# Optimization experiments

Measured on AMD Instinct MI355X. Metric: run time of the kernel, lower is better.

The kernel has to match this reference:

```python
import jax, jax.numpy as jnp
import numpy as np

B, D, N, M = 8, 256, 2048, 2048
H = 4
DH = D // H  # 64
EPS = 1e-5


def setup_inputs() -> dict:
    key = jax.random.key(0)
    ks = jax.random.split(key, 16)
    s = 0.05
    return {
        "x": jax.random.normal(ks[0], (B, D, N), jnp.float32),
        "source": jax.random.normal(ks[1], (B, D, M), jnp.float32),
        # per-head QKV projection weights (equivalent to H separate Conv1d(D, DH, 1))
        "Wq": jax.random.normal(ks[2], (H, DH, D), jnp.float32) * s,
        "bq": jax.random.normal(ks[3], (H, DH), jnp.float32) * s,
        "Wk": jax.random.normal(ks[4], (H, DH, D), jnp.float32) * s,
        "bk": jax.random.normal(ks[5], (H, DH), jnp.float32) * s,
        "Wv": jax.random.normal(ks[6], (H, DH, D), jnp.float32) * s,
        "bv": jax.random.normal(ks[7], (H, DH), jnp.float32) * s,
        # merge Conv1d(D, D, 1)
        "Wm": jax.random.normal(ks[8], (D, D), jnp.float32) * s,
        "bm": jax.random.normal(ks[9], (D,), jnp.float32) * s,
        # MLP: Conv1d(2D, 2D, 1) -> InstanceNorm -> ReLU -> Conv1d(2D, D, 1)
        "W1": jax.random.normal(ks[10], (2 * D, 2 * D), jnp.float32) * s,
        "b1": jax.random.normal(ks[11], (2 * D,), jnp.float32) * s,
        "W2": jax.random.normal(ks[12], (D, 2 * D), jnp.float32) * s,
        "b2": jnp.zeros((D,), jnp.float32),  # nn.init.constant_(mlp[-1].bias, 0.0)
    }


def reference(x, source, Wq, bq, Wk, bk, Wv, bv, Wm, bm, W1, b1, W2, b2):
    # Per-head 1x1-conv QKV projections, batched: [B, DH, H, N]
    q = jnp.einsum('bdn,hkd->bkhn', x, Wq) + bq.T[None, :, :, None]
    k = jnp.einsum('bdm,hkd->bkhm', source, Wk) + bk.T[None, :, :, None]
    v = jnp.einsum('bdm,hkd->bkhm', source, Wv) + bv.T[None, :, :, None]
    # scaled dot-product attention (scale = head dim)
    scores = jnp.einsum('bkhn,bkhm->bhnm', q, k) / jnp.sqrt(jnp.float32(DH))
    prob = jax.nn.softmax(scores, axis=-1)
    msg = jnp.einsum('bhnm,bkhm->bkhn', prob, v)
    # view(B, DH*H, N): dim-major then head, matches jnp reshape of [B, DH, H, N]
    msg = msg.reshape(B, DH * H, N)
    message = jnp.einsum('bcn,ec->ben', msg, Wm) + bm[None, :, None]
    # MLP on concat([x, message])
    h = jnp.concatenate([x, message], axis=1)  # [B, 2D, N]
    h = jnp.einsum('bcn,oc->bon', h, W1) + b1[None, :, None]
    # InstanceNorm1d (affine=False, biased variance, eps=1e-5) over N per (b, c)
    mean = jnp.mean(h, axis=-1, keepdims=True)
    var = jnp.var(h, axis=-1, keepdims=True)
    h = (h - mean) / jnp.sqrt(var + EPS)
    h = jax.nn.relu(h)
    out = jnp.einsum('bcn,oc->bon', h, W2) + b2[None, :, None]
    return out
```

## Files before the change

kernel.cpp:

```cpp
#include <hip/hip_runtime.h>
#include <hip/hip_bf16.h>

#define B_  8
#define D_  256
#define N_  2048
#define M_  2048
#define H_  4
#define DH_ 64
#define D2_ 512

#define SCL_QK 0.1803368801f

typedef unsigned short ushort_t;
typedef __attribute__((ext_vector_type(8))) short bf16x8;
typedef __attribute__((ext_vector_type(4))) short bf16x4;
typedef __attribute__((ext_vector_type(4))) float f32x4;

__device__ __forceinline__ unsigned cvtpk(float a, float b) {
  unsigned r;
  asm("v_cvt_pk_bf16_f32 %0, %1, %2" : "=v"(r) : "v"(a), "v"(b));
  return r;
}
__device__ __forceinline__ ushort_t f2bf1(float x) {
  return (ushort_t)cvtpk(x, x);
}
__device__ __forceinline__ float bf2f(ushort_t h) {
  union { unsigned u; float f; } c; c.u = ((unsigned)h) << 16; return c.f;
}
__device__ __forceinline__ uint2 pack4(float a, float b, float c, float d) {
  uint2 r; r.x = cvtpk(a, b); r.y = cvtpk(c, d); return r;
}

__device__ __forceinline__ void gload16(const ushort_t* g, ushort_t* l) {
  __builtin_amdgcn_global_load_lds(
      (const __attribute__((address_space(1))) unsigned*)g,
      (__attribute__((address_space(3))) unsigned*)l, 16, 0, 0);
}

template <int K, int LDB>
__device__ __forceinline__ void mfma_core(const ushort_t* __restrict__ Arow,
                                          const ushort_t* __restrict__ Brow,
                                          f32x4 acc[4][4], int lg) {
#pragma unroll 2
  for (int k0 = 0; k0 < K; k0 += 32) {
    bf16x8 af[4], bfr[4];
#pragma unroll
    for (int f = 0; f < 4; ++f)
      af[f] = *(const bf16x8*)&Arow[(size_t)16 * f * K + k0 + lg * 8];
#pragma unroll
    for (int f = 0; f < 4; ++f)
      bfr[f] = *(const bf16x8*)&Brow[(size_t)16 * f * LDB + k0 + lg * 8];
#pragma unroll
    for (int fm = 0; fm < 4; ++fm)
#pragma unroll
      for (int fn = 0; fn < 4; ++fn)
        acc[fm][fn] = __builtin_amdgcn_mfma_f32_16x16x32_bf16(
            af[fm], bfr[fn], acc[fm][fn], 0, 0, 0);
  }
}

#define GEMM_PREAMBLE()                                   \
  const int t = threadIdx.x, lane = t & 63, wv = t >> 6;  \
  const int wm = wv >> 1, wn = wv & 1;                    \
  const int lq = lane & 15, lg = lane >> 4;               \
  const int m0 = blockIdx.y * 128 + wm * 64;              \
  const int n0 = blockIdx.x * 128 + wn * 64;              \
  f32x4 acc[4][4];                                        \
  _Pragma("unroll") for (int i = 0; i < 4; ++i)           \
  _Pragma("unroll") for (int j = 0; j < 4; ++j)           \
      acc[i][j] = (f32x4){0.f, 0.f, 0.f, 0.f};

__global__ __launch_bounds__(256) void prep_weights(
    const float* __restrict__ Wq, const float* __restrict__ Wk,
    const float* __restrict__ Wv, const float* __restrict__ Wm,
    const float* __restrict__ W1, const float* __restrict__ W2,
    ushort_t* __restrict__ Wqb, ushort_t* __restrict__ Wkb,
    ushort_t* __restrict__ Wvb, ushort_t* __restrict__ Wmb,
    ushort_t* __restrict__ W1b, ushort_t* __restrict__ W2b) {
  const int idx = blockIdx.x * 256 + threadIdx.x;
  if (idx < 65536) {
    Wqb[idx] = f2bf1(Wq[idx] * SCL_QK);
  } else if (idx < 131072) {
    int j = idx - 65536; Wkb[j] = f2bf1(Wk[j]);
  } else if (idx < 196608) {
    int j = idx - 131072; Wvb[j] = f2bf1(Wv[j]);
  } else if (idx < 262144) {
    int j = idx - 196608;
    int e = j >> 8, cp = j & 255;
    int h = cp >> 6, dh = cp & 63;
    Wmb[j] = f2bf1(Wm[e * 256 + dh * 4 + h]);
  } else if (idx < 524288) {
    int j = idx - 262144; W1b[j] = f2bf1(W1[j]);
  } else if (idx < 655360) {
    int j = idx - 524288; W2b[j] = f2bf1(W2[j]);
  }
}

__global__ __launch_bounds__(256) void transpose_in(
    const float* __restrict__ x, const float* __restrict__ source,
    ushort_t* __restrict__ cat_t, ushort_t* __restrict__ st) {
  __shared__ float T[64][65];
  const int t = threadIdx.x;
  const int b = blockIdx.z & 7, which = blockIdx.z >> 3;
  const float* sb = (which ? source : x) + (size_t)b * D_ * N_;
  ushort_t* dst = which ? st + (size_t)b * N_ * 256 : cat_t + (size_t)b * N_ * 512;
  const int ldc = which ? 256 : 512;
  const int d0 = blockIdx.y * 64, n0 = blockIdx.x * 64;
  const int nn = t & 63, dd = t >> 6;
#pragma unroll
  for (int p = 0; p < 16; ++p)
    T[dd + 4 * p][nn] = sb[(size_t)(d0 + dd + 4 * p) * N_ + n0 + nn];
  __syncthreads();
  const int dg = t & 7, nr = t >> 3;
#pragma unroll
  for (int p = 0; p < 2; ++p) {
    int n = nr + 32 * p;
    uint4 pv;
    pv.x = cvtpk(T[dg * 8 + 0][n], T[dg * 8 + 1][n]);
    pv.y = cvtpk(T[dg * 8 + 2][n], T[dg * 8 + 3][n]);
    pv.z = cvtpk(T[dg * 8 + 4][n], T[dg * 8 + 5][n]);
    pv.w = cvtpk(T[dg * 8 + 6][n], T[dg * 8 + 7][n]);
    *(uint4*)&dst[(size_t)(n0 + n) * ldc + d0 + dg * 8] = pv;
  }
}

__global__ __launch_bounds__(256) void q_mfma(
    const ushort_t* __restrict__ Wqb, const float* __restrict__ bq,
    const ushort_t* __restrict__ cat_t, ushort_t* __restrict__ Qt) {
  GEMM_PREAMBLE()
  const int b = blockIdx.z;
  const ushort_t* Arow = Wqb + (size_t)(m0 + lq) * 256;
  const ushort_t* Brow = cat_t + ((size_t)b * N_ + n0 + lq) * 512;
  mfma_core<256, 512>(Arow, Brow, acc, lg);
  ushort_t* Qb = Qt + (size_t)b * 4 * N_ * 64;
#pragma unroll
  for (int fm = 0; fm < 4; ++fm) {
    const int o0 = m0 + 16 * fm + 4 * lg;
    const int hh = o0 >> 6, dl = o0 & 63;
    float bb[4];
#pragma unroll
    for (int r = 0; r < 4; ++r) bb[r] = bq[o0 + r] * SCL_QK;
#pragma unroll
    for (int fn = 0; fn < 4; ++fn) {
      const int n = n0 + 16 * fn + lq;
      uint2 pv = pack4(acc[fm][fn][0] + bb[0], acc[fm][fn][1] + bb[1],
                       acc[fm][fn][2] + bb[2], acc[fm][fn][3] + bb[3]);
      *(uint2*)&Qb[((size_t)hh * N_ + n) * 64 + dl] = pv;
    }
  }
}

__global__ __launch_bounds__(256) void kv_mfma(
    const ushort_t* __restrict__ Wkb, const ushort_t* __restrict__ Wvb,
    const float* __restrict__ bk, const float* __restrict__ bv,
    const ushort_t* __restrict__ st, ushort_t* __restrict__ Kt,
    ushort_t* __restrict__ Vt) {
  const int b = blockIdx.z >> 1, w = blockIdx.z & 1;
  GEMM_PREAMBLE()
  const ushort_t* A = w ? Wvb : Wkb;
  const float* bias = w ? bv : bk;
  const ushort_t* Arow = A + (size_t)(m0 + lq) * 256;
  const ushort_t* Brow = st + ((size_t)b * N_ + n0 + lq) * 256;
  mfma_core<256, 256>(Arow, Brow, acc, lg);
  if (w == 0) {
    ushort_t* Kb = Kt + (size_t)b * 4 * N_ * 64;
#pragma unroll
    for (int fm = 0; fm < 4; ++fm) {
      const int o0 = m0 + 16 * fm + 4 * lg;
      const int hh = o0 >> 6, dl = o0 & 63;
      float bb[4];
#pragma unroll
      for (int r = 0; r < 4; ++r) bb[r] = bias[o0 + r];
#pragma unroll
      for (int fn = 0; fn < 4; ++fn) {
        const int n = n0 + 16 * fn + lq;
        uint2 pv = pack4(acc[fm][fn][0] + bb[0], acc[fm][fn][1] + bb[1],
                         acc[fm][fn][2] + bb[2], acc[fm][fn][3] + bb[3]);
        *(uint2*)&Kb[((size_t)hh * N_ + n) * 64 + dl] = pv;
      }
    }
  } else {
    ushort_t* Vb = Vt + (size_t)b * 256 * N_;
#pragma unroll
    for (int fm = 0; fm < 4; ++fm) {
      const int o0 = m0 + 16 * fm + 4 * lg;
      float bb[4];
#pragma unroll
      for (int r = 0; r < 4; ++r) bb[r] = bias[o0 + r];
#pragma unroll
      for (int fn = 0; fn < 4; ++fn) {
        const int n = n0 + 16 * fn + lq;
#pragma unroll
        for (int r = 0; r < 4; ++r)
          Vb[(size_t)(o0 + r) * N_ + n] = f2bf1(acc[fm][fn][r] + bb[r]);
      }
    }
  }
}

__global__ __launch_bounds__(256) void attn_mfma(
    const ushort_t* __restrict__ Qt, const ushort_t* __restrict__ Kt,
    const ushort_t* __restrict__ Vt, ushort_t* __restrict__ msgT) {
  __shared__ __align__(16) ushort_t Ks[2 * 64 * 64];
  __shared__ __align__(16) ushort_t Vs[2 * 64 * 64];
  __shared__ __align__(16) ushort_t Ps[64 * 64];
  const int t = threadIdx.x;
  const int lane = t & 63, wq = t >> 6;
  const int flat = blockIdx.x;
  const int logical = (flat & 7) * 128 + (flat >> 3);
  const int qt = logical & 31, h = (logical >> 5) & 3, b = logical >> 7;
  const int bh = b * H_ + h;
  const size_t base = (size_t)bh * 64 * N_;
  const int n00 = qt * 64;
  const int lq = lane & 15, lg = lane >> 4;
  const int qrow = wq * 16 + lq;
  const int sw = (lq & 7) * 8;

  const int r0 = wq * 16 + (lane >> 3);
  const int r1 = r0 + 8;
  const int c8 = lane & 7;
  const ushort_t* kp0 = Kt + base + (size_t)r0 * 64 + ((c8 ^ (r0 & 7)) * 8);
  const ushort_t* kp1 = Kt + base + (size_t)r1 * 64 + ((c8 ^ (r1 & 7)) * 8);
  const ushort_t* vp0 = Vt + base + (size_t)r0 * N_ + ((c8 ^ (r0 & 7)) * 8);
  const ushort_t* vp1 = Vt + base + (size_t)r1 * N_ + ((c8 ^ (r1 & 7)) * 8);
  const int wbase = wq * 1024;

  bf16x8 qf0, qf1;
  {
    const ushort_t* qp = Qt + base + (size_t)(n00 + qrow) * 64 + lg * 8;
    qf0 = *(const bf16x8*)qp;
    qf1 = *(const bf16x8*)(qp + 32);
  }
  f32x4 o0 = {0.f, 0.f, 0.f, 0.f}, o1 = o0, o2 = o0, o3 = o0;
  float lrun = 0.f;

  gload16(kp0, &Ks[wbase]);
  gload16(kp1, &Ks[wbase + 512]);
  gload16(vp0, &Vs[wbase]);
  gload16(vp1, &Vs[wbase + 512]);
  kp0 += 4096; kp1 += 4096; vp0 += 64; vp1 += 64;
  __syncthreads();

  int cur = 0;
  for (int tile = 0; tile < 32; ++tile) {
    if (tile != 31) {
      const int nb = (cur ^ 1) * 4096;
      gload16(kp0, &Ks[nb + wbase]);
      gload16(kp1, &Ks[nb + wbase + 512]);
      gload16(vp0, &Vs[nb + wbase]);
      gload16(vp1, &Vs[nb + wbase + 512]);
      kp0 += 4096; kp1 += 4096; vp0 += 64; vp1 += 64;
    }
    const int kb = cur * 4096;

    f32x4 s0 = {0.f, 0.f, 0.f, 0.f}, s1 = s0, s2 = s0, s3 = s0;
#pragma unroll
    for (int kt = 0; kt < 2; ++kt) {
      const int dh0 = ((lg * 8 + 32 * kt) ^ sw) + kb;
      const bf16x8 qb = kt ? qf1 : qf0;
      s0 = __builtin_amdgcn_mfma_f32_16x16x32_bf16(
          *(const bf16x8*)&Ks[lq * 64 + dh0], qb, s0, 0, 0, 0);
      s1 = __builtin_amdgcn_mfma_f32_16x16x32_bf16(
          *(const bf16x8*)&Ks[(16 + lq) * 64 + dh0], qb, s1, 0, 0, 0);
      s2 = __builtin_amdgcn_mfma_f32_16x16x32_bf16(
          *(const bf16x8*)&Ks[(32 + lq) * 64 + dh0], qb, s2, 0, 0, 0);
      s3 = __builtin_amdgcn_mfma_f32_16x16x32_bf16(
          *(const bf16x8*)&Ks[(48 + lq) * 64 + dh0], qb, s3, 0, 0, 0);
    }

    float ls = 0.f;
#define PSTORE(SF, KF)                                                    \
    {                                                                     \
      float e0 = exp2f(SF[0]), e1 = exp2f(SF[1]);                         \
      float e2 = exp2f(SF[2]), e3 = exp2f(SF[3]);                         \
      ls += (e0 + e1) + (e2 + e3);                                        \
      uint2 pv;                                                           \
      pv.x = cvtpk(e0, e1);                                               \
      pv.y = cvtpk(e2, e3);                                               \
      *(uint2*)&Ps[qrow * 64 + ((16 * (KF) + 4 * lg) ^ sw)] = pv;         \
    }
    PSTORE(s0, 0) PSTORE(s1, 1) PSTORE(s2, 2) PSTORE(s3, 3)
#undef PSTORE
    lrun += ls;
    asm volatile("s_waitcnt lgkmcnt(0)" ::: "memory");
    __builtin_amdgcn_sched_barrier(0);

#pragma unroll
    for (int kt = 0; kt < 2; ++kt) {
      const int k0 = (lg * 8 + 32 * kt) ^ sw;
      const bf16x8 pb = *(const bf16x8*)&Ps[qrow * 64 + k0];
      o0 = __builtin_amdgcn_mfma_f32_16x16x32_bf16(
          *(const bf16x8*)&Vs[lq * 64 + k0 + kb], pb, o0, 0, 0, 0);
      o1 = __builtin_amdgcn_mfma_f32_16x16x32_bf16(
          *(const bf16x8*)&Vs[(16 + lq) * 64 + k0 + kb], pb, o1, 0, 0, 0);
      o2 = __builtin_amdgcn_mfma_f32_16x16x32_bf16(
          *(const bf16x8*)&Vs[(32 + lq) * 64 + k0 + kb], pb, o2, 0, 0, 0);
      o3 = __builtin_amdgcn_mfma_f32_16x16x32_bf16(
          *(const bf16x8*)&Vs[(48 + lq) * 64 + k0 + kb], pb, o3, 0, 0, 0);
    }
    __syncthreads();
    cur ^= 1;
  }

  lrun += __shfl_xor(lrun, 16);
  lrun += __shfl_xor(lrun, 32);
  const float inv = 1.f / lrun;

  ushort_t* mp = msgT + ((size_t)b * N_ + n00 + qrow) * 256 + h * 64;
  uint2 pv;
  pv = pack4(o0[0] * inv, o0[1] * inv, o0[2] * inv, o0[3] * inv);
  *(uint2*)&mp[0 + 4 * lg] = pv;
  pv = pack4(o1[0] * inv, o1[1] * inv, o1[2] * inv, o1[3] * inv);
  *(uint2*)&mp[16 + 4 * lg] = pv;
  pv = pack4(o2[0] * inv, o2[1] * inv, o2[2] * inv, o2[3] * inv);
  *(uint2*)&mp[32 + 4 * lg] = pv;
  pv = pack4(o3[0] * inv, o3[1] * inv, o3[2] * inv, o3[3] * inv);
  *(uint2*)&mp[48 + 4 * lg] = pv;
}

__global__ __launch_bounds__(256) void merge_mfma(
    const ushort_t* __restrict__ Wmb, const float* __restrict__ bm,
    const ushort_t* __restrict__ msgT, ushort_t* __restrict__ cat_t) {
  GEMM_PREAMBLE()
  const int b = blockIdx.z;
  const ushort_t* Arow = Wmb + (size_t)(m0 + lq) * 256;
  const ushort_t* Brow = msgT + ((size_t)b * N_ + n0 + lq) * 256;
  mfma_core<256, 256>(Arow, Brow, acc, lg);
  ushort_t* ob = cat_t + (size_t)b * N_ * 512 + 256;
#pragma unroll
  for (int fm = 0; fm < 4; ++fm) {
    const int o0 = m0 + 16 * fm + 4 * lg;
    float bb[4];
#pragma unroll
    for (int r = 0; r < 4; ++r) bb[r] = bm[o0 + r];
#pragma unroll
    for (int fn = 0; fn < 4; ++fn) {
      const int n = n0 + 16 * fn + lq;
      uint2 pv = pack4(acc[fm][fn][0] + bb[0], acc[fm][fn][1] + bb[1],
                       acc[fm][fn][2] + bb[2], acc[fm][fn][3] + bb[3]);
      *(uint2*)&ob[(size_t)n * 512 + o0] = pv;
    }
  }
}

__global__ __launch_bounds__(256) void w1_mfma(
    const ushort_t* __restrict__ W1b, const float* __restrict__ b1,
    const ushort_t* __restrict__ cat_t, ushort_t* __restrict__ h1t) {
  GEMM_PREAMBLE()
  const int b = blockIdx.z;
  const ushort_t* Arow = W1b + (size_t)(m0 + lq) * 512;
  const ushort_t* Brow = cat_t + ((size_t)b * N_ + n0 + lq) * 512;
  mfma_core<512, 512>(Arow, Brow, acc, lg);
  ushort_t* ob = h1t + (size_t)b * N_ * 512;
#pragma unroll
  for (int fm = 0; fm < 4; ++fm) {
    const int o0 = m0 + 16 * fm + 4 * lg;
    float bb[4];
#pragma unroll
    for (int r = 0; r < 4; ++r) bb[r] = b1[o0 + r];
#pragma unroll
    for (int fn = 0; fn < 4; ++fn) {
      const int n = n0 + 16 * fn + lq;
      uint2 pv = pack4(acc[fm][fn][0] + bb[0], acc[fm][fn][1] + bb[1],
                       acc[fm][fn][2] + bb[2], acc[fm][fn][3] + bb[3]);
      *(uint2*)&ob[(size_t)n * 512 + o0] = pv;
    }
  }
}

__global__ __launch_bounds__(256) void zero_stats(float* __restrict__ s) {
  s[blockIdx.x * 256 + threadIdx.x] = 0.f;
}

__global__ __launch_bounds__(256) void stats_partial(
    const ushort_t* __restrict__ h1t, float* __restrict__ ssum,
    float* __restrict__ ssq) {
  const int t = threadIdx.x;
  const int c = blockIdx.y * 64 + (t & 63);
  const int b = blockIdx.z;
  const int nbase = blockIdx.x * 256 + (t >> 6) * 64;
  const ushort_t* p = h1t + (size_t)b * N_ * 512;
  float s = 0.f, ss = 0.f;
  for (int i = 0; i < 64; ++i) {
    float v = bf2f(p[(size_t)(nbase + i) * 512 + c]);
    s += v; ss += v * v;
  }
  __shared__ float rs[4][64], rq[4][64];
  const int wv = t >> 6;
  rs[wv][t & 63] = s; rq[wv][t & 63] = ss;
  __syncthreads();
  if (t < 64) {
    float S = rs[0][t] + rs[1][t] + rs[2][t] + rs[3][t];
    float Q = rq[0][t] + rq[1][t] + rq[2][t] + rq[3][t];
    atomicAdd(&ssum[b * 512 + blockIdx.y * 64 + t], S);
    atomicAdd(&ssq[b * 512 + blockIdx.y * 64 + t], Q);
  }
}

__global__ __launch_bounds__(256) void finalize_stats(
    const float* __restrict__ ssum, const float* __restrict__ ssq,
    float* __restrict__ mean, float* __restrict__ istd) {
  const int i = blockIdx.x * 256 + threadIdx.x;
  float mn = ssum[i] * (1.f / N_);
  float var = ssq[i] * (1.f / N_) - mn * mn;
  mean[i] = mn;
  istd[i] = rsqrtf(var + 1e-5f);
}

__global__ __launch_bounds__(256) void normalize_h1(
    const ushort_t* __restrict__ h1t, const float* __restrict__ mean,
    const float* __restrict__ istd, ushort_t* __restrict__ h1n) {
  const size_t ci = (size_t)blockIdx.x * 256 + threadIdx.x;
  const size_t basei = ci * 8;
  const int c0 = (int)(basei & 511);
  const size_t row = basei >> 9;
  const int b = (int)(row >> 11);
  const float* mp = mean + b * 512 + c0;
  const float* ip = istd + b * 512 + c0;
  union { bf16x8 v; ushort_t u[8]; } in;
  in.v = *(const bf16x8*)&h1t[basei];
  float g[8];
#pragma unroll
  for (int j = 0; j < 8; ++j)
    g[j] = fmaxf((bf2f(in.u[j]) - mp[j]) * ip[j], 0.f);
  uint4 pv;
  pv.x = cvtpk(g[0], g[1]);
  pv.y = cvtpk(g[2], g[3]);
  pv.z = cvtpk(g[4], g[5]);
  pv.w = cvtpk(g[6], g[7]);
  *(uint4*)&h1n[basei] = pv;
}

__global__ __launch_bounds__(256) void w2_mfma(
    const ushort_t* __restrict__ W2b, const float* __restrict__ b2,
    const ushort_t* __restrict__ h1n, float* __restrict__ out) {
  GEMM_PREAMBLE()
  const int b = blockIdx.z;
  const ushort_t* Arow = W2b + (size_t)(m0 + lq) * 512;
  const ushort_t* Brow = h1n + ((size_t)b * N_ + n0 + lq) * 512;
  mfma_core<512, 512>(Arow, Brow, acc, lg);
  float* ob = out + (size_t)b * D_ * N_;
#pragma unroll
  for (int fm = 0; fm < 4; ++fm) {
    const int o0 = m0 + 16 * fm + 4 * lg;
    float bb[4];
#pragma unroll
    for (int r = 0; r < 4; ++r) bb[r] = b2[o0 + r];
#pragma unroll
    for (int fn = 0; fn < 4; ++fn) {
      const int n = n0 + 16 * fn + lq;
#pragma unroll
      for (int r = 0; r < 4; ++r)
        ob[(size_t)(o0 + r) * N_ + n] = acc[fm][fn][r] + bb[r];
    }
  }
}

extern "C" void kernel_launch(void* const* d_in, const int* in_sizes, int n_in,
                              void* d_out, int out_size, void* d_ws,
                              size_t ws_size, hipStream_t stream) {
  const float* x = (const float*)d_in[0];
  const float* source = (const float*)d_in[1];
  const float* Wq = (const float*)d_in[2];
  const float* bq = (const float*)d_in[3];
  const float* Wk = (const float*)d_in[4];
  const float* bk = (const float*)d_in[5];
  const float* Wv = (const float*)d_in[6];
  const float* bv = (const float*)d_in[7];
  const float* Wm = (const float*)d_in[8];
  const float* bm = (const float*)d_in[9];
  const float* W1 = (const float*)d_in[10];
  const float* b1 = (const float*)d_in[11];
  const float* W2 = (const float*)d_in[12];
  const float* b2 = (const float*)d_in[13];
  float* out = (float*)d_out;

  char* w = (char*)d_ws;
  size_t off = 0;
  auto alloc = [&](size_t bytes) {
    void* p = w + off;
    off = (off + bytes + 255) & ~(size_t)255;
    return p;
  };
  ushort_t* cat_t = (ushort_t*)alloc((size_t)B_ * N_ * 512 * 2);
  ushort_t* st    = (ushort_t*)alloc((size_t)B_ * N_ * 256 * 2);
  ushort_t* Qt    = (ushort_t*)alloc((size_t)B_ * 4 * N_ * 64 * 2);
  ushort_t* Kt    = (ushort_t*)alloc((size_t)B_ * 4 * N_ * 64 * 2);
  ushort_t* Vt    = (ushort_t*)alloc((size_t)B_ * 256 * N_ * 2);
  ushort_t* msgT  = (ushort_t*)alloc((size_t)B_ * N_ * 256 * 2);
  ushort_t* h1t   = (ushort_t*)alloc((size_t)B_ * N_ * 512 * 2);
  ushort_t* h1n   = (ushort_t*)alloc((size_t)B_ * N_ * 512 * 2);
  float* ssum = (float*)alloc(4096 * 4);
  float* ssq  = (float*)alloc(4096 * 4);
  float* mean = (float*)alloc(4096 * 4);
  float* istd = (float*)alloc(4096 * 4);
  ushort_t* Wqb = (ushort_t*)alloc(65536 * 2);
  ushort_t* Wkb = (ushort_t*)alloc(65536 * 2);
  ushort_t* Wvb = (ushort_t*)alloc(65536 * 2);
  ushort_t* Wmb = (ushort_t*)alloc(65536 * 2);
  ushort_t* W1b = (ushort_t*)alloc(262144 * 2);
  ushort_t* W2b = (ushort_t*)alloc(131072 * 2);

  prep_weights<<<2560, 256, 0, stream>>>(Wq, Wk, Wv, Wm, W1, W2, Wqb, Wkb,
                                         Wvb, Wmb, W1b, W2b);
  transpose_in<<<dim3(32, 4, 16), 256, 0, stream>>>(x, source, cat_t, st);
  zero_stats<<<32, 256, 0, stream>>>(ssum);
  q_mfma<<<dim3(16, 2, 8), 256, 0, stream>>>(Wqb, bq, cat_t, Qt);
  kv_mfma<<<dim3(16, 2, 16), 256, 0, stream>>>(Wkb, Wvb, bk, bv, st, Kt, Vt);
  attn_mfma<<<dim3(1024), 256, 0, stream>>>(Qt, Kt, Vt, msgT);
  merge_mfma<<<dim3(16, 2, 8), 256, 0, stream>>>(Wmb, bm, msgT, cat_t);
  w1_mfma<<<dim3(16, 4, 8), 256, 0, stream>>>(W1b, b1, cat_t, h1t);
  stats_partial<<<dim3(8, 8, 8), 256, 0, stream>>>(h1t, ssum, ssq);
  finalize_stats<<<16, 256, 0, stream>>>(ssum, ssq, mean, istd);
  normalize_h1<<<4096, 256, 0, stream>>>(h1t, mean, istd, h1n);
  w2_mfma<<<dim3(16, 2, 8), 256, 0, stream>>>(W2b, b2, h1n, out);
}
```

Before: 286.9 us.

## Fuse QKV projections and move instance-norm statistics into W1 GEMM epilogue

Merges the Q and KV projection kernels into one launch, folds stats zeroing into the weight prep kernel, and computes per-channel sum and sum-of-squares inside the W1 GEMM epilogue via shuffles and atomics. The finalize step is folded into the normalize kernel. This removes several kernel launches and a full re-read of the h1 activation. It adds atomic traffic per block and computes statistics from fp32 values rather than the rounded bf16 ones.

```diff
diff --git a/kernel.cpp b/kernel.cpp
--- a/kernel.cpp
+++ b/kernel.cpp
@@ -70,13 +70,14 @@
   _Pragma("unroll") for (int j = 0; j < 4; ++j)           \
       acc[i][j] = (f32x4){0.f, 0.f, 0.f, 0.f};
 
-__global__ __launch_bounds__(256) void prep_weights(
+__global__ __launch_bounds__(256) void prep_kernel(
     const float* __restrict__ Wq, const float* __restrict__ Wk,
     const float* __restrict__ Wv, const float* __restrict__ Wm,
     const float* __restrict__ W1, const float* __restrict__ W2,
     ushort_t* __restrict__ Wqb, ushort_t* __restrict__ Wkb,
     ushort_t* __restrict__ Wvb, ushort_t* __restrict__ Wmb,
-    ushort_t* __restrict__ W1b, ushort_t* __restrict__ W2b) {
+    ushort_t* __restrict__ W1b, ushort_t* __restrict__ W2b,
+    float* __restrict__ stats) {
   const int idx = blockIdx.x * 256 + threadIdx.x;
   if (idx < 65536) {
     Wqb[idx] = f2bf1(Wq[idx] * SCL_QK);
@@ -93,6 +94,9 @@
     int j = idx - 262144; W1b[j] = f2bf1(W1[j]);
   } else if (idx < 655360) {
     int j = idx - 524288; W2b[j] = f2bf1(W2[j]);
+  } else {
+    int j = idx - 655360;
+    if (j < 8192) stats[j] = 0.f;
   }
 }
 
@@ -124,53 +128,48 @@
   }
 }
 
-__global__ __launch_bounds__(256) void q_mfma(
-    const ushort_t* __restrict__ Wqb, const float* __restrict__ bq,
-    const ushort_t* __restrict__ cat_t, ushort_t* __restrict__ Qt) {
+__global__ __launch_bounds__(256) void qkv_mfma(
+    const ushort_t* __restrict__ Wqb, const ushort_t* __restrict__ Wkb,
+    const ushort_t* __restrict__ Wvb, const float* __restrict__ bq,
+    const float* __restrict__ bk, const float* __restrict__ bv,
+    const ushort_t* __restrict__ cat_t, const ushort_t* __restrict__ st,
+    ushort_t* __restrict__ Qt, ushort_t* __restrict__ Kt,
+    ushort_t* __restrict__ Vt) {
+  const int z = blockIdx.z;
+  const int b = z / 3, w = z % 3;
   GEMM_PREAMBLE()
-  const int b = blockIdx.z;
-  const ushort_t* Arow = Wqb + (size_t)(m0 + lq) * 256;
-  const ushort_t* Brow = cat_t + ((size_t)b * N_ + n0 + lq) * 512;
-  mfma_core<256, 512>(Arow, Brow, acc, lg);
-  ushort_t* Qb = Qt + (size_t)b * 4 * N_ * 64;
-#pragma unroll
-  for (int fm = 0; fm < 4; ++fm) {
-    const int o0 = m0 + 16 * fm + 4 * lg;
-    const int hh = o0 >> 6, dl = o0 & 63;
-    float bb[4];
-#pragma unroll
-    for (int r = 0; r < 4; ++r) bb[r] = bq[o0 + r] * SCL_QK;
-#pragma unroll
-    for (int fn = 0; fn < 4; ++fn) {
-      const int n = n0 + 16 * fn + lq;
-      uint2 pv = pack4(acc[fm][fn][0] + bb[0], acc[fm][fn][1] + bb[1],
-                       acc[fm][fn][2] + bb[2], acc[fm][fn][3] + bb[3]);
-      *(uint2*)&Qb[((size_t)hh * N_ + n) * 64 + dl] = pv;
-    }
-  }
-}
-
-__global__ __launch_bounds__(256) void kv_mfma(
-    const ushort_t* __restrict__ Wkb, const ushort_t* __restrict__ Wvb,
-    const float* __restrict__ bk, const float* __restrict__ bv,
-    const ushort_t* __restrict__ st, ushort_t* __restrict__ Kt,
-    ushort_t* __restrict__ Vt) {
-  const int b = blockIdx.z >> 1, w = blockIdx.z & 1;
-  GEMM_PREAMBLE()
-  const ushort_t* A = w ? Wvb : Wkb;
-  const float* bias = w ? bv : bk;
-  const ushort_t* Arow = A + (size_t)(m0 + lq) * 256;
-  const ushort_t* Brow = st + ((size_t)b * N_ + n0 + lq) * 256;
-  mfma_core<256, 256>(Arow, Brow, acc, lg);
   if (w == 0) {
-    ushort_t* Kb = Kt + (size_t)b * 4 * N_ * 64;
+    const ushort_t* Arow = Wqb + (size_t)(m0 + lq) * 256;
+    const ushort_t* Brow = cat_t + ((size_t)b * N_ + n0 + lq) * 512;
+    mfma_core<256, 512>(Arow, Brow, acc, lg);
+    ushort_t* Qb = Qt + (size_t)b * 4 * N_ * 64;
 #pragma unroll
     for (int fm = 0; fm < 4; ++fm) {
       const int o0 = m0 + 16 * fm + 4 * lg;
       const int hh = o0 >> 6, dl = o0 & 63;
       float bb[4];
 #pragma unroll
-      for (int r = 0; r < 4; ++r) bb[r] = bias[o0 + r];
+      for (int r = 0; r < 4; ++r) bb[r] = bq[o0 + r] * SCL_QK;
+#pragma unroll
+      for (int fn = 0; fn < 4; ++fn) {
+        const int n = n0 + 16 * fn + lq;
+        uint2 pv = pack4(acc[fm][fn][0] + bb[0], acc[fm][fn][1] + bb[1],
+                         acc[fm][fn][2] + bb[2], acc[fm][fn][3] + bb[3]);
+        *(uint2*)&Qb[((size_t)hh * N_ + n) * 64 + dl] = pv;
+      }
+    }
+  } else if (w == 1) {
+    const ushort_t* Arow = Wkb + (size_t)(m0 + lq) * 256;
+    const ushort_t* Brow = st + ((size_t)b * N_ + n0 + lq) * 256;
+    mfma_core<256, 256>(Arow, Brow, acc, lg);
+    ushort_t* Kb = Kt + (size_t)b * 4 * N_ * 64;
+#pragma unroll
+    for (int fm = 0; fm < 4; ++fm) {
+      const int o0 = m0 + 16 * fm + 4 * lg;
+      const int hh = o0 >> 6, dl = o0 & 63;
+      float bb[4];
+#pragma unroll
+      for (int r = 0; r < 4; ++r) bb[r] = bk[o0 + r];
 #pragma unroll
       for (int fn = 0; fn < 4; ++fn) {
         const int n = n0 + 16 * fn + lq;
@@ -180,13 +179,16 @@
       }
     }
   } else {
+    const ushort_t* Arow = Wvb + (size_t)(m0 + lq) * 256;
+    const ushort_t* Brow = st + ((size_t)b * N_ + n0 + lq) * 256;
+    mfma_core<256, 256>(Arow, Brow, acc, lg);
     ushort_t* Vb = Vt + (size_t)b * 256 * N_;
 #pragma unroll
     for (int fm = 0; fm < 4; ++fm) {
       const int o0 = m0 + 16 * fm + 4 * lg;
       float bb[4];
 #pragma unroll
-      for (int r = 0; r < 4; ++r) bb[r] = bias[o0 + r];
+      for (int r = 0; r < 4; ++r) bb[r] = bv[o0 + r];
 #pragma unroll
       for (int fn = 0; fn < 4; ++fn) {
         const int n = n0 + 16 * fn + lq;
@@ -345,7 +347,8 @@
 
 __global__ __launch_bounds__(256) void w1_mfma(
     const ushort_t* __restrict__ W1b, const float* __restrict__ b1,
-    const ushort_t* __restrict__ cat_t, ushort_t* __restrict__ h1t) {
+    const ushort_t* __restrict__ cat_t, ushort_t* __restrict__ h1t,
+    float* __restrict__ ssum, float* __restrict__ ssq) {
   GEMM_PREAMBLE()
   const int b = blockIdx.z;
   const ushort_t* Arow = W1b + (size_t)(m0 + lq) * 512;
@@ -360,69 +363,59 @@
     for (int r = 0; r < 4; ++r) bb[r] = b1[o0 + r];
 #pragma unroll
     for (int fn = 0; fn < 4; ++fn) {
+#pragma unroll
+      for (int r = 0; r < 4; ++r) acc[fm][fn][r] += bb[r];
       const int n = n0 + 16 * fn + lq;
-      uint2 pv = pack4(acc[fm][fn][0] + bb[0], acc[fm][fn][1] + bb[1],
-                       acc[fm][fn][2] + bb[2], acc[fm][fn][3] + bb[3]);
+      uint2 pv = pack4(acc[fm][fn][0], acc[fm][fn][1], acc[fm][fn][2],
+                       acc[fm][fn][3]);
       *(uint2*)&ob[(size_t)n * 512 + o0] = pv;
     }
   }
-}
-
-__global__ __launch_bounds__(256) void zero_stats(float* __restrict__ s) {
-  s[blockIdx.x * 256 + threadIdx.x] = 0.f;
-}
-
-__global__ __launch_bounds__(256) void stats_partial(
-    const ushort_t* __restrict__ h1t, float* __restrict__ ssum,
-    float* __restrict__ ssq) {
-  const int t = threadIdx.x;
-  const int c = blockIdx.y * 64 + (t & 63);
-  const int b = blockIdx.z;
-  const int nbase = blockIdx.x * 256 + (t >> 6) * 64;
-  const ushort_t* p = h1t + (size_t)b * N_ * 512;
-  float s = 0.f, ss = 0.f;
-  for (int i = 0; i < 64; ++i) {
-    float v = bf2f(p[(size_t)(nbase + i) * 512 + c]);
-    s += v; ss += v * v;
-  }
-  __shared__ float rs[4][64], rq[4][64];
-  const int wv = t >> 6;
-  rs[wv][t & 63] = s; rq[wv][t & 63] = ss;
-  __syncthreads();
-  if (t < 64) {
-    float S = rs[0][t] + rs[1][t] + rs[2][t] + rs[3][t];
-    float Q = rq[0][t] + rq[1][t] + rq[2][t] + rq[3][t];
-    atomicAdd(&ssum[b * 512 + blockIdx.y * 64 + t], S);
-    atomicAdd(&ssq[b * 512 + blockIdx.y * 64 + t], Q);
-  }
-}
-
-__global__ __launch_bounds__(256) void finalize_stats(
-    const float* __restrict__ ssum, const float* __restrict__ ssq,
-    float* __restrict__ mean, float* __restrict__ istd) {
-  const int i = blockIdx.x * 256 + threadIdx.x;
-  float mn = ssum[i] * (1.f / N_);
-  float var = ssq[i] * (1.f / N_) - mn * mn;
-  mean[i] = mn;
-  istd[i] = rsqrtf(var + 1e-5f);
+#pragma unroll
+  for (int fm = 0; fm < 4; ++fm) {
+#pragma unroll
+    for (int r = 0; r < 4; ++r) {
+      float sv = 0.f, qv = 0.f;
+#pragma unroll
+      for (int fn = 0; fn < 4; ++fn) {
+        float v = acc[fm][fn][r];
+        sv += v;
+        qv += v * v;
+      }
+#pragma unroll
+      for (int off = 1; off < 16; off <<= 1) {
+        sv += __shfl_xor(sv, off);
+        qv += __shfl_xor(qv, off);
+      }
+      if (lq == 0) {
+        const int o = m0 + 16 * fm + 4 * lg + r;
+        atomicAdd(&ssum[b * 512 + o], sv);
+        atomicAdd(&ssq[b * 512 + o], qv);
+      }
+    }
+  }
 }
 
 __global__ __launch_bounds__(256) void normalize_h1(
-    const ushort_t* __restrict__ h1t, const float* __restrict__ mean,
-    const float* __restrict__ istd, ushort_t* __restrict__ h1n) {
+    const ushort_t* __restrict__ h1t, const float* __restrict__ ssum,
+    const float* __restrict__ ssq, ushort_t* __restrict__ h1n) {
   const size_t ci = (size_t)blockIdx.x * 256 + threadIdx.x;
   const size_t basei = ci * 8;
   const int c0 = (int)(basei & 511);
   const size_t row = basei >> 9;
   const int b = (int)(row >> 11);
-  const float* mp = mean + b * 512 + c0;
-  const float* ip = istd + b * 512 + c0;
+  const float* sp = ssum + b * 512 + c0;
+  const float* qp = ssq + b * 512 + c0;
   union { bf16x8 v; ushort_t u[8]; } in;
   in.v = *(const bf16x8*)&h1t[basei];
   float g[8];
 #pragma unroll
-  for (int j = 0; j < 8; ++j)
-    g[j] = fmaxf((bf2f(in.u[j]) - mp[j]) * ip[j], 0.f);
+  for (int j = 0; j < 8; ++j) {
+    float mn = sp[j] * (1.f / N_);
+    float var = qp[j] * (1.f / N_) - mn * mn;
+    float istd = rsqrtf(var + 1e-5f);
+    g[j] = fmaxf((bf2f(in.u[j]) - mn) * istd, 0.f);
+  }
   uint4 pv;
   pv.x = cvtpk(g[0], g[1]);
   pv.y = cvtpk(g[2], g[3]);
@@ -492,8 +485,6 @@
   ushort_t* h1n   = (ushort_t*)alloc((size_t)B_ * N_ * 512 * 2);
   float* ssum = (float*)alloc(4096 * 4);
   float* ssq  = (float*)alloc(4096 * 4);
-  float* mean = (float*)alloc(4096 * 4);
-  float* istd = (float*)alloc(4096 * 4);
   ushort_t* Wqb = (ushort_t*)alloc(65536 * 2);
   ushort_t* Wkb = (ushort_t*)alloc(65536 * 2);
   ushort_t* Wvb = (ushort_t*)alloc(65536 * 2);
@@ -501,17 +492,14 @@
   ushort_t* W1b = (ushort_t*)alloc(262144 * 2);
   ushort_t* W2b = (ushort_t*)alloc(131072 * 2);
 
-  prep_weights<<<2560, 256, 0, stream>>>(Wq, Wk, Wv, Wm, W1, W2, Wqb, Wkb,
-                                         Wvb, Wmb, W1b, W2b);
+  prep_kernel<<<2592, 256, 0, stream>>>(Wq, Wk, Wv, Wm, W1, W2, Wqb, Wkb, Wvb,
+                                        Wmb, W1b, W2b, ssum);
   transpose_in<<<dim3(32, 4, 16), 256, 0, stream>>>(x, source, cat_t, st);
-  zero_stats<<<32, 256, 0, stream>>>(ssum);
-  q_mfma<<<dim3(16, 2, 8), 256, 0, stream>>>(Wqb, bq, cat_t, Qt);
-  kv_mfma<<<dim3(16, 2, 16), 256, 0, stream>>>(Wkb, Wvb, bk, bv, st, Kt, Vt);
+  qkv_mfma<<<dim3(16, 2, 24), 256, 0, stream>>>(Wqb, Wkb, Wvb, bq, bk, bv,
+                                                cat_t, st, Qt, Kt, Vt);
   attn_mfma<<<dim3(1024), 256, 0, stream>>>(Qt, Kt, Vt, msgT);
   merge_mfma<<<dim3(16, 2, 8), 256, 0, stream>>>(Wmb, bm, msgT, cat_t);
-  w1_mfma<<<dim3(16, 4, 8), 256, 0, stream>>>(W1b, b1, cat_t, h1t);
-  stats_partial<<<dim3(8, 8, 8), 256, 0, stream>>>(h1t, ssum, ssq);
-  finalize_stats<<<16, 256, 0, stream>>>(ssum, ssq, mean, istd);
-  normalize_h1<<<4096, 256, 0, stream>>>(h1t, mean, istd, h1n);
+  w1_mfma<<<dim3(16, 4, 8), 256, 0, stream>>>(W1b, b1, cat_t, h1t, ssum, ssq);
+  normalize_h1<<<4096, 256, 0, stream>>>(h1t, ssum, ssq, h1n);
   w2_mfma<<<dim3(16, 2, 8), 256, 0, stream>>>(W2b, b2, h1n, out);
 }
```

After: 285.0 us. Within noise of the previous version (-0.6%).
